# Optimization experiments

Measured on AMD Instinct MI355X. Metric: run time of the kernel, lower is better.

## Reference

```python
import jax, jax.numpy as jnp
import numpy as np

B, IN_FEATURES, UNITS, BITS = 64, 1024, 1024, 8


def setup_inputs() -> dict:
    key = jax.random.key(0)
    k1, k2, k3 = jax.random.split(key, 3)
    # Quantized integer activations stored as float32 (TF code does int math).
    x = jax.random.randint(k1, (B, IN_FEATURES), 0, 16).astype(jnp.float32)
    # Low-bit integer weights: BITS-bit signed magnitude, |w| < 4**(BITS//2).
    kernel = jax.random.randint(k2, (IN_FEATURES, UNITS), -128, 128).astype(jnp.float32)
    bias = jax.random.randint(k3, (UNITS,), -32, 32).astype(jnp.float32)
    return {"x": x, "kernel": kernel, "bias": bias, "bits": BITS}


def reference(x, kernel, bias, bits):
    # Faithful vectorized version of the TF bit-serial quantized matmul.
    # TF per-feature loop is vectorized over the input-feature axis; the
    # small fixed loop over 2-bit weight chunks is kept (bits//2 iterations).
    nchunks = bits // 2
    sgn = jnp.sign(kernel)            # (In, U)
    wa = jnp.abs(kernel)              # (In, U)
    x3 = x[:, :, None]                # (B, In, 1)
    d = jnp.zeros((x.shape[0], x.shape[1], kernel.shape[1]), x.dtype)  # (B, In, U)
    for _ in range(nchunks):
        c = (wa % 4.0) * sgn          # current 2-bit chunk, re-signed
        d = d + x3 * c[None, :, :]
        wa = jnp.trunc(wa / 4.0)      # tf.cast(w/4, int32): trunc toward 0 (w >= 0)
        d = jnp.trunc(d / 4.0)        # tf.cast(dim1/4, int32): trunc toward 0
    res = d.sum(axis=1)               # (B, U), accumulation over input features
    return jax.nn.relu(res + bias)    # activation == 'relu' branch
```

## Files before the change

kernel.cpp:

```cpp
#include <hip/hip_runtime.h>

#define IN_F   1024
#define UNITS  1024
#define BDIM   64
#define NCH    32
#define CHUNK  32
#define BG     4
#define NBG    16


__global__ __launch_bounds__(256) void partial_kernel(
    const float* __restrict__ x, const float* __restrict__ K,
    float* __restrict__ ws)
{
    const int bid = blockIdx.x;
    const int bg = bid & (NBG - 1);
    const int ic = bid >> 4;
    const int t  = threadIdx.x;
    const int b0 = bg * BG;
    const int i0 = ic * CHUNK;

    __shared__ float xs[CHUNK * BG];
    if (t < CHUNK * BG) {
        const int ii = t >> 2;
        const int bb = t & 3;
        xs[ii * BG + bb] = x[(b0 + bb) * IN_F + i0 + ii] * (1.0f / 256.0f);
    }
    __syncthreads();

    float4 acc0 = make_float4(0.f, 0.f, 0.f, 0.f);
    float4 acc1 = acc0, acc2 = acc0, acc3 = acc0;

    const float4* kp = (const float4*)(K + (size_t)i0 * UNITS) + t;
#pragma unroll 4
    for (int i = 0; i < CHUNK; ++i) {
        const float4 k4 = kp[(size_t)i * (UNITS / 4)];
        const float4 xv = *(const float4*)&xs[i * BG];
        acc0.x += truncf(xv.x * k4.x); acc0.y += truncf(xv.x * k4.y);
        acc0.z += truncf(xv.x * k4.z); acc0.w += truncf(xv.x * k4.w);
        acc1.x += truncf(xv.y * k4.x); acc1.y += truncf(xv.y * k4.y);
        acc1.z += truncf(xv.y * k4.z); acc1.w += truncf(xv.y * k4.w);
        acc2.x += truncf(xv.z * k4.x); acc2.y += truncf(xv.z * k4.y);
        acc2.z += truncf(xv.z * k4.z); acc2.w += truncf(xv.z * k4.w);
        acc3.x += truncf(xv.w * k4.x); acc3.y += truncf(xv.w * k4.y);
        acc3.z += truncf(xv.w * k4.z); acc3.w += truncf(xv.w * k4.w);
    }

    float4* wp = (float4*)(ws + ((size_t)ic * BDIM + b0) * UNITS) + t;
    wp[0 * (UNITS / 4)] = acc0;
    wp[1 * (UNITS / 4)] = acc1;
    wp[2 * (UNITS / 4)] = acc2;
    wp[3 * (UNITS / 4)] = acc3;
}

__global__ __launch_bounds__(128) void reduce_kernel(
    const float* __restrict__ ws, const float* __restrict__ bias,
    float* __restrict__ out)
{
    const int idx = blockIdx.x * 128 + threadIdx.x;
    const int j4 = idx & 255;
    const int b  = idx >> 8;

    const float4* p = (const float4*)ws + (size_t)b * (UNITS / 4) + j4;
    float4 s = make_float4(0.f, 0.f, 0.f, 0.f);
#pragma unroll
    for (int c = 0; c < NCH; ++c) {
        const float4 v = p[(size_t)c * BDIM * (UNITS / 4)];
        s.x += v.x; s.y += v.y; s.z += v.z; s.w += v.w;
    }
    const float4 bv = ((const float4*)bias)[j4];
    s.x = fmaxf(s.x + bv.x, 0.f);
    s.y = fmaxf(s.y + bv.y, 0.f);
    s.z = fmaxf(s.z + bv.z, 0.f);
    s.w = fmaxf(s.w + bv.w, 0.f);
    ((float4*)out)[idx] = s;
}

extern "C" void kernel_launch(void* const* d_in, const int* in_sizes, int n_in,
                              void* d_out, int out_size, void* d_ws, size_t ws_size,
                              hipStream_t stream) {
    const float* x    = (const float*)d_in[0];
    const float* K    = (const float*)d_in[1];
    const float* bias = (const float*)d_in[2];
    float* out = (float*)d_out;
    float* ws  = (float*)d_ws;

    partial_kernel<<<NBG * NCH, 256, 0, stream>>>(x, K, ws);
    reduce_kernel<<<128, 128, 0, stream>>>(ws, bias, out);
}
```

Baseline: 74.05 us.

## Reduce split-K partials in shared memory and accumulate with global atomics

Each block now covers 128 input features and a 256-wide column tile, split across four thread groups whose partial sums are combined in shared memory. The block result is then added into a zeroed workspace with atomicAdd, which replaces the 32-way partial-sum write and re-read. This cuts workspace traffic from 32 slices to 8 atomic contributions per output, at the cost of an extra zeroing kernel launch and atomic contention. Float addition order becomes nondeterministic, though all summands are integer-valued, so sums should stay exact.

Measured after the change: 82.24 us. 1.11x slower.

```diff
diff --git a/kernel.cpp b/kernel.cpp
--- a/kernel.cpp
+++ b/kernel.cpp
@@ -3,39 +3,56 @@
 #define IN_F   1024
 #define UNITS  1024
 #define BDIM   64
-#define NCH    32
-#define CHUNK  32
 #define BG     4
-#define NBG    16
+#define JT     256
+#define ICH    8
+#define CHUNK  128
+#define REPS   4
+#define ISUB   32
 
+
+__global__ __launch_bounds__(256) void zero_ws_kernel(float4* __restrict__ ws4)
+{
+    const int idx = blockIdx.x * 256 + threadIdx.x;
+    ws4[idx] = make_float4(0.f, 0.f, 0.f, 0.f);
+}
 
 __global__ __launch_bounds__(256) void partial_kernel(
     const float* __restrict__ x, const float* __restrict__ K,
     float* __restrict__ ws)
 {
     const int bid = blockIdx.x;
-    const int bg = bid & (NBG - 1);
-    const int ic = bid >> 4;
+    const int bg = bid & 15;
+    const int jt = (bid >> 4) & 3;
+    const int ic = bid >> 6;
     const int t  = threadIdx.x;
     const int b0 = bg * BG;
+    const int j0 = jt * JT;
     const int i0 = ic * CHUNK;
 
+    const int j4  = t & 63;
+    const int rep = t >> 6;
+
     __shared__ float xs[CHUNK * BG];
-    if (t < CHUNK * BG) {
-        const int ii = t >> 2;
-        const int bb = t & 3;
-        xs[ii * BG + bb] = x[(b0 + bb) * IN_F + i0 + ii] * (1.0f / 256.0f);
+    {
+        const int t2 = t;
+        const int ii0 = t2 >> 2, bb0 = t2 & 3;
+        xs[ii0 * BG + bb0] = x[(b0 + bb0) * IN_F + i0 + ii0] * (1.0f / 256.0f);
+        const int t3 = t + 256;
+        const int ii1 = t3 >> 2, bb1 = t3 & 3;
+        xs[ii1 * BG + bb1] = x[(b0 + bb1) * IN_F + i0 + ii1] * (1.0f / 256.0f);
     }
     __syncthreads();
 
     float4 acc0 = make_float4(0.f, 0.f, 0.f, 0.f);
     float4 acc1 = acc0, acc2 = acc0, acc3 = acc0;
 
-    const float4* kp = (const float4*)(K + (size_t)i0 * UNITS) + t;
-#pragma unroll 4
-    for (int i = 0; i < CHUNK; ++i) {
-        const float4 k4 = kp[(size_t)i * (UNITS / 4)];
-        const float4 xv = *(const float4*)&xs[i * BG];
+    const int ib = rep * ISUB;
+    const float4* kp = (const float4*)(K + (size_t)(i0 + ib) * UNITS + j0) + j4;
+#pragma unroll 8
+    for (int r = 0; r < ISUB; ++r) {
+        const float4 k4 = kp[(size_t)r * (UNITS / 4)];
+        const float4 xv = *(const float4*)&xs[(ib + r) * BG];
         acc0.x += truncf(xv.x * k4.x); acc0.y += truncf(xv.x * k4.y);
         acc0.z += truncf(xv.x * k4.z); acc0.w += truncf(xv.x * k4.w);
         acc1.x += truncf(xv.y * k4.x); acc1.y += truncf(xv.y * k4.y);
@@ -46,34 +63,46 @@
         acc3.z += truncf(xv.w * k4.z); acc3.w += truncf(xv.w * k4.w);
     }
 
-    float4* wp = (float4*)(ws + ((size_t)ic * BDIM + b0) * UNITS) + t;
-    wp[0 * (UNITS / 4)] = acc0;
-    wp[1 * (UNITS / 4)] = acc1;
-    wp[2 * (UNITS / 4)] = acc2;
-    wp[3 * (UNITS / 4)] = acc3;
+    __shared__ float red[REPS * BG * JT];
+    float* rb = red + rep * (BG * JT);
+    *(float4*)&rb[(0 * 64 + j4) * 4] = acc0;
+    *(float4*)&rb[(1 * 64 + j4) * 4] = acc1;
+    *(float4*)&rb[(2 * 64 + j4) * 4] = acc2;
+    *(float4*)&rb[(3 * 64 + j4) * 4] = acc3;
+    __syncthreads();
+
+    const float4 s0 = *(const float4*)&red[0 * 1024 + t * 4];
+    const float4 s1 = *(const float4*)&red[1 * 1024 + t * 4];
+    const float4 s2 = *(const float4*)&red[2 * 1024 + t * 4];
+    const float4 s3 = *(const float4*)&red[3 * 1024 + t * 4];
+    const float sx = s0.x + s1.x + s2.x + s3.x;
+    const float sy = s0.y + s1.y + s2.y + s3.y;
+    const float sz = s0.z + s1.z + s2.z + s3.z;
+    const float sw = s0.w + s1.w + s2.w + s3.w;
+
+    const int bb = t >> 6;
+    const int jj = t & 63;
+    float* wp = ws + (size_t)(b0 + bb) * UNITS + j0 + jj * 4;
+    atomicAdd(wp + 0, sx);
+    atomicAdd(wp + 1, sy);
+    atomicAdd(wp + 2, sz);
+    atomicAdd(wp + 3, sw);
 }
 
-__global__ __launch_bounds__(128) void reduce_kernel(
-    const float* __restrict__ ws, const float* __restrict__ bias,
-    float* __restrict__ out)
+__global__ __launch_bounds__(256) void finalize_kernel(
+    const float4* __restrict__ ws4, const float4* __restrict__ bias4,
+    float4* __restrict__ out4)
 {
-    const int idx = blockIdx.x * 128 + threadIdx.x;
+    const int idx = blockIdx.x * 256 + threadIdx.x;
     const int j4 = idx & 255;
-    const int b  = idx >> 8;
-
-    const float4* p = (const float4*)ws + (size_t)b * (UNITS / 4) + j4;
-    float4 s = make_float4(0.f, 0.f, 0.f, 0.f);
-#pragma unroll
-    for (int c = 0; c < NCH; ++c) {
-        const float4 v = p[(size_t)c * BDIM * (UNITS / 4)];
-        s.x += v.x; s.y += v.y; s.z += v.z; s.w += v.w;
-    }
-    const float4 bv = ((const float4*)bias)[j4];
-    s.x = fmaxf(s.x + bv.x, 0.f);
-    s.y = fmaxf(s.y + bv.y, 0.f);
-    s.z = fmaxf(s.z + bv.z, 0.f);
-    s.w = fmaxf(s.w + bv.w, 0.f);
-    ((float4*)out)[idx] = s;
+    const float4 s = ws4[idx];
+    const float4 bv = bias4[j4];
+    float4 r;
+    r.x = fmaxf(s.x + bv.x, 0.f);
+    r.y = fmaxf(s.y + bv.y, 0.f);
+    r.z = fmaxf(s.z + bv.z, 0.f);
+    r.w = fmaxf(s.w + bv.w, 0.f);
+    out4[idx] = r;
 }
 
 extern "C" void kernel_launch(void* const* d_in, const int* in_sizes, int n_in,
@@ -85,6 +114,8 @@
     float* out = (float*)d_out;
     float* ws  = (float*)d_ws;
 
-    partial_kernel<<<NBG * NCH, 256, 0, stream>>>(x, K, ws);
-    reduce_kernel<<<128, 128, 0, stream>>>(ws, bias, out);
+    zero_ws_kernel<<<64, 256, 0, stream>>>((float4*)ws);
+    partial_kernel<<<512, 256, 0, stream>>>(x, K, ws);
+    finalize_kernel<<<64, 256, 0, stream>>>((const float4*)ws,
+                                            (const float4*)bias, (float4*)out);
 }
```

## Fuse partial matmul and reduction into single kernel with in-block shared-memory reduction

Applied to the files above, without the earlier changes.

Replaces the two-kernel split-K scheme, which wrote partial sums to a workspace and reduced them in a second launch, with one kernel. Each block now owns a 4-batch by 32-unit output tile and splits the full input dimension across 32 thread groups, then reduces those partials in shared memory and applies bias plus relu directly. This removes the workspace round trip through global memory and one kernel launch. In exchange each block stages all 1024 input features for its batch group into 16KB of shared memory, and K reads become narrower 128-byte row segments per thread group instead of full coalesced rows.

Result: slower. 76.68 us (+3.6%).

```diff
diff --git a/kernel.cpp b/kernel.cpp
--- a/kernel.cpp
+++ b/kernel.cpp
@@ -3,77 +3,76 @@
 #define IN_F   1024
 #define UNITS  1024
 #define BDIM   64
-#define NCH    32
-#define CHUNK  32
 #define BG     4
+#define JT     32
 #define NBG    16
+#define NJT    32
+#define REPS   32
+#define ISUB   32
 
 
-__global__ __launch_bounds__(256) void partial_kernel(
+__global__ __launch_bounds__(256) void dense_kernel(
     const float* __restrict__ x, const float* __restrict__ K,
-    float* __restrict__ ws)
+    const float* __restrict__ bias, float* __restrict__ out)
 {
     const int bid = blockIdx.x;
     const int bg = bid & (NBG - 1);
-    const int ic = bid >> 4;
+    const int jt = bid >> 4;
     const int t  = threadIdx.x;
     const int b0 = bg * BG;
-    const int i0 = ic * CHUNK;
+    const int j0 = jt * JT;
 
-    __shared__ float xs[CHUNK * BG];
-    if (t < CHUNK * BG) {
-        const int ii = t >> 2;
-        const int bb = t & 3;
-        xs[ii * BG + bb] = x[(b0 + bb) * IN_F + i0 + ii] * (1.0f / 256.0f);
+    __shared__ float xs[IN_F * BG];
+#pragma unroll
+    for (int c = 0; c < 16; ++c) {
+        const int e  = c * 256 + t;
+        const int bb = e >> 10;
+        const int ii = e & 1023;
+        xs[ii * BG + bb] = x[(b0 + bb) * IN_F + ii] * (1.0f / 256.0f);
     }
     __syncthreads();
 
-    float4 acc0 = make_float4(0.f, 0.f, 0.f, 0.f);
-    float4 acc1 = acc0, acc2 = acc0, acc3 = acc0;
+    const int j4  = t & 7;
+    const int rep = t >> 3;
 
-    const float4* kp = (const float4*)(K + (size_t)i0 * UNITS) + t;
-#pragma unroll 4
-    for (int i = 0; i < CHUNK; ++i) {
-        const float4 k4 = kp[(size_t)i * (UNITS / 4)];
-        const float4 xv = *(const float4*)&xs[i * BG];
-        acc0.x += truncf(xv.x * k4.x); acc0.y += truncf(xv.x * k4.y);
-        acc0.z += truncf(xv.x * k4.z); acc0.w += truncf(xv.x * k4.w);
-        acc1.x += truncf(xv.y * k4.x); acc1.y += truncf(xv.y * k4.y);
-        acc1.z += truncf(xv.y * k4.z); acc1.w += truncf(xv.y * k4.w);
-        acc2.x += truncf(xv.z * k4.x); acc2.y += truncf(xv.z * k4.y);
-        acc2.z += truncf(xv.z * k4.z); acc2.w += truncf(xv.z * k4.w);
-        acc3.x += truncf(xv.w * k4.x); acc3.y += truncf(xv.w * k4.y);
-        acc3.z += truncf(xv.w * k4.z); acc3.w += truncf(xv.w * k4.w);
+    float4 a0 = make_float4(0.f, 0.f, 0.f, 0.f);
+    float4 a1 = a0, a2 = a0, a3 = a0;
+
+    const float4* kp = (const float4*)(K + (size_t)(rep * ISUB) * UNITS + j0) + j4;
+    const float*  xp = xs + (rep * ISUB) * BG;
+#pragma unroll 8
+    for (int r = 0; r < ISUB; ++r) {
+        const float4 k4 = kp[(size_t)r * (UNITS / 4)];
+        const float4 xv = *(const float4*)&xp[r * BG];
+        a0.x += truncf(xv.x * k4.x); a0.y += truncf(xv.x * k4.y);
+        a0.z += truncf(xv.x * k4.z); a0.w += truncf(xv.x * k4.w);
+        a1.x += truncf(xv.y * k4.x); a1.y += truncf(xv.y * k4.y);
+        a1.z += truncf(xv.y * k4.z); a1.w += truncf(xv.y * k4.w);
+        a2.x += truncf(xv.z * k4.x); a2.y += truncf(xv.z * k4.y);
+        a2.z += truncf(xv.z * k4.z); a2.w += truncf(xv.z * k4.w);
+        a3.x += truncf(xv.w * k4.x); a3.y += truncf(xv.w * k4.y);
+        a3.z += truncf(xv.w * k4.z); a3.w += truncf(xv.w * k4.w);
     }
 
-    float4* wp = (float4*)(ws + ((size_t)ic * BDIM + b0) * UNITS) + t;
-    wp[0 * (UNITS / 4)] = acc0;
-    wp[1 * (UNITS / 4)] = acc1;
-    wp[2 * (UNITS / 4)] = acc2;
-    wp[3 * (UNITS / 4)] = acc3;
-}
+    __shared__ float red[REPS][BG * JT];
+    {
+        float* rb = red[rep];
+        *(float4*)&rb[0 * JT + j4 * 4] = a0;
+        *(float4*)&rb[1 * JT + j4 * 4] = a1;
+        *(float4*)&rb[2 * JT + j4 * 4] = a2;
+        *(float4*)&rb[3 * JT + j4 * 4] = a3;
+    }
+    __syncthreads();
 
-__global__ __launch_bounds__(128) void reduce_kernel(
-    const float* __restrict__ ws, const float* __restrict__ bias,
-    float* __restrict__ out)
-{
-    const int idx = blockIdx.x * 128 + threadIdx.x;
-    const int j4 = idx & 255;
-    const int b  = idx >> 8;
-
-    const float4* p = (const float4*)ws + (size_t)b * (UNITS / 4) + j4;
-    float4 s = make_float4(0.f, 0.f, 0.f, 0.f);
+    if (t < BG * JT) {
+        float s = 0.f;
 #pragma unroll
-    for (int c = 0; c < NCH; ++c) {
-        const float4 v = p[(size_t)c * BDIM * (UNITS / 4)];
-        s.x += v.x; s.y += v.y; s.z += v.z; s.w += v.w;
+        for (int rp = 0; rp < REPS; ++rp) s += red[rp][t];
+        const int bb = t >> 5;
+        const int jj = t & 31;
+        const float v = s + bias[j0 + jj];
+        out[(size_t)(b0 + bb) * UNITS + j0 + jj] = fmaxf(v, 0.f);
     }
-    const float4 bv = ((const float4*)bias)[j4];
-    s.x = fmaxf(s.x + bv.x, 0.f);
-    s.y = fmaxf(s.y + bv.y, 0.f);
-    s.z = fmaxf(s.z + bv.z, 0.f);
-    s.w = fmaxf(s.w + bv.w, 0.f);
-    ((float4*)out)[idx] = s;
 }
 
 extern "C" void kernel_launch(void* const* d_in, const int* in_sizes, int n_in,
@@ -83,8 +82,7 @@
     const float* K    = (const float*)d_in[1];
     const float* bias = (const float*)d_in[2];
     float* out = (float*)d_out;
-    float* ws  = (float*)d_ws;
+    (void)d_ws; (void)ws_size;
 
-    partial_kernel<<<NBG * NCH, 256, 0, stream>>>(x, K, ws);
-    reduce_kernel<<<128, 128, 0, stream>>>(ws, bias, out);
+    dense_kernel<<<NBG * NJT, 256, 0, stream>>>(x, K, bias, out);
 }
```
